# Kernel tuning notes

Hardware: AMD Instinct MI355X
Metric: run time of the kernel (lower is better)

## Reference

```python
import jax, jax.numpy as jnp
import numpy as np

B, H, L, D, S = 4, 16, 4096, 64, 128

def setup_inputs() -> dict:
    key = jax.random.key(0)
    k1, k2 = jax.random.split(key)
    x = jax.random.normal(k1, (B, H, L, D), dtype=jnp.float32)
    c = jax.random.normal(k2, (H, S, D), dtype=jnp.float32)
    # codebook rows are unit-normalized at init (matches torch init)
    c = c / jnp.linalg.norm(c, axis=-1, keepdims=True)
    return {"x": x, "c": c}

def reference(x, c):
    # cosine-similarity scores: [B,H,L,S]
    cos_sim = jnp.einsum('bhld,hsd->bhls', x, c)
    delta_index = jnp.argmax(cos_sim, axis=-1)            # [B,H,L]
    delta_onehot = jax.nn.one_hot(delta_index, c.shape[-2], dtype=jnp.float32)  # [B,H,L,S]
    return (delta_onehot, c)
```

## Files before the change

kernel.cpp:

```cpp
#include <hip/hip_runtime.h>
#include <math.h>

constexpr int BB = 4;
constexpr int HH = 16;
constexpr int LL = 4096;
constexpr int DD = 64;
constexpr int SS = 128;
constexpr int WR = 16;

constexpr float TAU = 2e-3f;

typedef __attribute__((ext_vector_type(8))) short bf16x8;
typedef __attribute__((ext_vector_type(4))) float f32x4;

#define MFMA16 __builtin_amdgcn_mfma_f32_16x16x32_bf16

__device__ __forceinline__ unsigned short f2bf(float v) {
    unsigned u = __float_as_uint(v);
    return (unsigned short)((u + 0x7fffu + ((u >> 16) & 1u)) >> 16);
}

__device__ __forceinline__ void split8(const float4 va, const float4 vb,
                                       uint4* hi, uint4* lo) {
    const float v[8] = {va.x, va.y, va.z, va.w, vb.x, vb.y, vb.z, vb.w};
    unsigned hw[4], lw[4];
    #pragma unroll
    for (int p = 0; p < 4; ++p) {
        const unsigned u0 = __float_as_uint(v[2 * p]);
        const unsigned u1 = __float_as_uint(v[2 * p + 1]);
        const unsigned h0 = u0 & 0xffff0000u;
        const unsigned h1 = u1 & 0xffff0000u;
        hw[p] = (u0 >> 16) | h1;
        lw[p] = (unsigned)f2bf(v[2 * p] - __uint_as_float(h0))
              | ((unsigned)f2bf(v[2 * p + 1] - __uint_as_float(h1)) << 16);
    }
    *hi = make_uint4(hw[0], hw[1], hw[2], hw[3]);
    *lo = make_uint4(lw[0], lw[1], lw[2], lw[3]);
}

union FragU { uint4 q; bf16x8 v; };

__global__ __launch_bounds__(256) void convert_c_kernel(
    const float* __restrict__ c, unsigned char* __restrict__ ws,
    float* __restrict__ out_c)
{
    const int sid = blockIdx.x * 256 + threadIdx.x;
    if (sid == 0) *(int*)(ws + (size_t)HH * 32768) = 0;
    const int h  = sid >> 10;
    const int r  = sid & 1023;
    const int kt = r >> 9;
    const int ct = (r >> 6) & 7;
    const int ln = r & 63;
    const int cc = ct * 16 + (ln & 15);
    const int k0 = kt * 32 + (ln >> 4) * 8;
    const float4* src = (const float4*)(c + ((size_t)h * SS + cc) * DD + k0);
    uint4 hi, lo;
    split8(src[0], src[1], &hi, &lo);
    unsigned char* base =
        ws + (size_t)h * 32768 + (size_t)(((kt << 3) | ct) * 1024 + ln * 16);
    *(uint4*)(base) = hi;
    *(uint4*)(base + 16384) = lo;

    const f32x4* __restrict__ s4 = (const f32x4*)c;
    f32x4* __restrict__ d4 = (f32x4*)out_c;
    __builtin_nontemporal_store(s4[sid], d4 + sid);
    __builtin_nontemporal_store(s4[sid + 16384], d4 + sid + 16384);
}

template <bool USE_WS>
__global__ __launch_bounds__(64, 8) void quantizer_kernel(
    const float* __restrict__ x,
    const float* __restrict__ c,
    const unsigned char* __restrict__ ws,
    float* __restrict__ out,
    int* __restrict__ gcount,
    int* __restrict__ glist)
{
    __shared__ int s_res[WR];

    const int lane = threadIdx.x;
    const int ln15 = lane & 15;
    const long long r0 = (long long)blockIdx.x * WR;
    const int h = (int)((r0 >> 12) & (HH - 1));
    const unsigned char* __restrict__ wsb =
        USE_WS ? (ws + (size_t)h * 32768) : nullptr;
    const float* __restrict__ chead = c + (size_t)h * SS * DD;
    const int k0 = (lane >> 4) * 8;

    bf16x8 af[2][2];
    {
        const float* xr = x + (size_t)(r0 + ln15) * DD + k0;
        #pragma unroll
        for (int kt = 0; kt < 2; ++kt) {
            FragU hi, lo;
            split8(*(const float4*)(xr + kt * 32),
                   *(const float4*)(xr + kt * 32 + 4), &hi.q, &lo.q);
            af[kt][0] = hi.v;
            af[kt][1] = lo.v;
        }
    }

    float m1[4], m2[4];
    int   mi_[4];
    #pragma unroll
    for (int r = 0; r < 4; ++r) {
        m1[r] = -INFINITY; m2[r] = -INFINITY; mi_[r] = 0;
    }

    #pragma unroll 1
    for (int ct = 0; ct < 8; ++ct) {
        f32x4 a0 = {0.f, 0.f, 0.f, 0.f};
        f32x4 a1 = {0.f, 0.f, 0.f, 0.f};
        if constexpr (USE_WS) {
            const unsigned char* bp = wsb + (unsigned)(ct * 1024 + lane * 16);
            {
                const bf16x8 bh = *(const bf16x8*)(bp);
                const bf16x8 bl = *(const bf16x8*)(bp + 16384);
                a0 = MFMA16(af[0][1], bh, a0, 0, 0, 0);
                a0 = MFMA16(af[0][0], bl, a0, 0, 0, 0);
                a0 = MFMA16(af[0][0], bh, a0, 0, 0, 0);
            }
            {
                const bf16x8 bh = *(const bf16x8*)(bp + 8192);
                const bf16x8 bl = *(const bf16x8*)(bp + 24576);
                a1 = MFMA16(af[1][1], bh, a1, 0, 0, 0);
                a1 = MFMA16(af[1][0], bl, a1, 0, 0, 0);
                a1 = MFMA16(af[1][0], bh, a1, 0, 0, 0);
            }
        } else {
            const float* cr = chead + (size_t)(ct * 16 + ln15) * DD + k0;
            {
                FragU bh, bl;
                split8(*(const float4*)cr, *(const float4*)(cr + 4),
                       &bh.q, &bl.q);
                a0 = MFMA16(af[0][1], bh.v, a0, 0, 0, 0);
                a0 = MFMA16(af[0][0], bl.v, a0, 0, 0, 0);
                a0 = MFMA16(af[0][0], bh.v, a0, 0, 0, 0);
            }
            {
                FragU bh, bl;
                split8(*(const float4*)(cr + 32), *(const float4*)(cr + 36),
                       &bh.q, &bl.q);
                a1 = MFMA16(af[1][1], bh.v, a1, 0, 0, 0);
                a1 = MFMA16(af[1][0], bl.v, a1, 0, 0, 0);
                a1 = MFMA16(af[1][0], bh.v, a1, 0, 0, 0);
            }
        }
        #pragma unroll
        for (int r = 0; r < 4; ++r) {
            const float v = a0[r] + a1[r];
            const int col = ct * 16 + ln15;
            m2[r] = __builtin_amdgcn_fmed3f(m1[r], v, m2[r]);
            if (v > m1[r]) { m1[r] = v; mi_[r] = col; }
        }
    }

    {
        int rv[4];
        #pragma unroll
        for (int r = 0; r < 4; ++r) {
            float a1 = m1[r], a2 = m2[r];
            int ai = mi_[r];
            #pragma unroll
            for (int off = 1; off <= 8; off <<= 1) {
                const float o1 = __shfl_xor(a1, off);
                const float o2 = __shfl_xor(a2, off);
                const int   oi = __shfl_xor(ai, off);
                const bool take = (o1 > a1) || (o1 == a1 && oi < ai);
                const float n2 = take ? fmaxf(a1, o2) : fmaxf(a2, o1);
                if (take) { a1 = o1; ai = oi; }
                a2 = n2;
            }
            rv[r] = ai;
            if (ln15 == 0 && (a1 - a2) < TAU) {
                const int row = (lane >> 4) * 4 + r;
                const int p = atomicAdd(gcount, 1);
                glist[p] = (int)(r0 + row);
            }
        }
        if (ln15 == 0)
            *(int4*)&s_res[(lane >> 4) * 4] =
                make_int4(rv[0], rv[1], rv[2], rv[3]);
    }

    f32x4* __restrict__ op = (f32x4*)(out + (size_t)r0 * SS);
    #pragma unroll
    for (int k = 0; k < 8; ++k) {
        const int i = lane + k * 64;
        const int am = s_res[i >> 5];
        const int s0 = (i & 31) * 4;
        f32x4 v = {(s0 + 0 == am) ? 1.f : 0.f,
                   (s0 + 1 == am) ? 1.f : 0.f,
                   (s0 + 2 == am) ? 1.f : 0.f,
                   (s0 + 3 == am) ? 1.f : 0.f};
        __builtin_nontemporal_store(v, op + i);
    }
}

__global__ __launch_bounds__(64) void fixup_kernel(
    const float* __restrict__ x, const float* __restrict__ c,
    const int* __restrict__ gcount, const int* __restrict__ glist,
    float* __restrict__ out)
{
    const int lane = threadIdx.x;
    const int cnt = *gcount;
    for (int idx = blockIdx.x; idx < cnt; idx += gridDim.x) {
        const int row = glist[idx];
        const int h = (row >> 12) & (HH - 1);
        const float* __restrict__ chead = c + (size_t)h * SS * DD;
        const float4* __restrict__ xr = (const float4*)(x + (size_t)row * DD);
        const float4* __restrict__ c0 =
            (const float4*)(chead + (size_t)lane * DD);
        const float4* __restrict__ c1 =
            (const float4*)(chead + (size_t)(lane + 64) * DD);
        float s0 = 0.f, s1 = 0.f;
        #pragma unroll
        for (int q = 0; q < 16; ++q) {
            const float4 a = xr[q];
            const float4 b0 = c0[q];
            const float4 b1 = c1[q];
            s0 = fmaf(a.x, b0.x, s0); s0 = fmaf(a.y, b0.y, s0);
            s0 = fmaf(a.z, b0.z, s0); s0 = fmaf(a.w, b0.w, s0);
            s1 = fmaf(a.x, b1.x, s1); s1 = fmaf(a.y, b1.y, s1);
            s1 = fmaf(a.z, b1.z, s1); s1 = fmaf(a.w, b1.w, s1);
        }
        float v = s0; int bi = lane;
        if (s1 > v) { v = s1; bi = lane + 64; }
        #pragma unroll
        for (int off = 1; off < 64; off <<= 1) {
            const float ov = __shfl_xor(v, off);
            const int   oi = __shfl_xor(bi, off);
            if (ov > v || (ov == v && oi < bi)) { v = ov; bi = oi; }
        }
        f32x4* __restrict__ op = (f32x4*)(out + (size_t)row * SS);
        if (lane < 32) {
            const int s0c = lane * 4;
            f32x4 w = {(s0c + 0 == bi) ? 1.f : 0.f,
                       (s0c + 1 == bi) ? 1.f : 0.f,
                       (s0c + 2 == bi) ? 1.f : 0.f,
                       (s0c + 3 == bi) ? 1.f : 0.f};
            op[lane] = w;
        }
    }
}

extern "C" void kernel_launch(void* const* d_in, const int* in_sizes, int n_in,
                              void* d_out, int out_size, void* d_ws, size_t ws_size,
                              hipStream_t stream) {
    const float* x = (const float*)d_in[0];
    const float* c = (const float*)d_in[1];
    float* out = (float*)d_out;
    float* out_c = out + (size_t)BB * HH * LL * SS;

    const int rows = BB * HH * LL;
    const int blocks = rows / WR;
    const size_t wsB = (size_t)HH * 32768;
    const size_t ws_need = wsB + 64 + (size_t)rows * 4;

    if (d_ws != nullptr && ws_size >= ws_need) {
        unsigned char* wsp = (unsigned char*)d_ws;
        int* gcount = (int*)(wsp + wsB);
        int* glist = (int*)(wsp + wsB + 64);
        convert_c_kernel<<<64, 256, 0, stream>>>(c, wsp, out_c);
        quantizer_kernel<true><<<blocks, 64, 0, stream>>>(
            x, c, wsp, out, gcount, glist);
        fixup_kernel<<<256, 64, 0, stream>>>(x, c, gcount, glist, out);
    } else {
        static int dummy = 0;
        (void)dummy;
        unsigned char* wsp = (unsigned char*)d_ws;
        if (wsp == nullptr || ws_size < 64 + (size_t)rows * 4) {
            fixup_kernel<<<2048, 64, 0, stream>>>(x, c, nullptr, nullptr, out);
            return;
        }
        int* gcount = (int*)wsp;
        int* glist = (int*)(wsp + 64);
        convert_c_kernel<<<64, 256, 0, stream>>>(c, (unsigned char*)wsp, out_c);
        quantizer_kernel<false><<<blocks, 64, 0, stream>>>(
            x, c, nullptr, out, gcount, glist);
        fixup_kernel<<<256, 64, 0, stream>>>(x, c, gcount, glist, out);
    }
}
```

Baseline: 213.1 us.

## Stage codebook in LDS and double-buffer x rows via async global-to-LDS loads

The quantizer kernel now uses 256-thread blocks, each handling 8 groups of 64 rows. The per-head bf16 hi/lo codebook is loaded once into shared memory, so each wave no longer re-reads it from global memory. The x rows are double-buffered into LDS with global_load_lds and an explicit vmcnt wait, so the next group's loads overlap the MFMA and argmax work on the current group. In exchange, far fewer blocks are launched and each uses about 64KB of LDS, which limits occupancy; the hand-placed waitcnt and sched barriers also rely on the exact count of outstanding loads.

```diff
diff --git a/kernel.cpp b/kernel.cpp
--- a/kernel.cpp
+++ b/kernel.cpp
@@ -7,6 +7,8 @@
 constexpr int DD = 64;
 constexpr int SS = 128;
 constexpr int WR = 16;
+constexpr int NW = 4;
+constexpr int NG = 8;
 
 constexpr float TAU = 2e-3f;
 
@@ -68,7 +70,7 @@
 }
 
 template <bool USE_WS>
-__global__ __launch_bounds__(64, 8) void quantizer_kernel(
+__global__ __launch_bounds__(256) void quantizer_kernel(
     const float* __restrict__ x,
     const float* __restrict__ c,
     const unsigned char* __restrict__ ws,
@@ -76,43 +78,99 @@
     int* __restrict__ gcount,
     int* __restrict__ glist)
 {
-    __shared__ int s_res[WR];
-
-    const int lane = threadIdx.x;
+    __shared__ __align__(16) unsigned char smemB[32768];
+    __shared__ __align__(16) unsigned char xstage[NW * 8192];
+    __shared__ int s_res[NW][WR];
+
+    const int tid = threadIdx.x;
+    const int wv = tid >> 6;
+    const int lane = tid & 63;
     const int ln15 = lane & 15;
-    const long long r0 = (long long)blockIdx.x * WR;
-    const int h = (int)((r0 >> 12) & (HH - 1));
-    const unsigned char* __restrict__ wsb =
-        USE_WS ? (ws + (size_t)h * 32768) : nullptr;
+    const long long R0 = (long long)blockIdx.x * (WR * NW * NG);
+    const int h = (int)((R0 >> 12) & (HH - 1));
     const float* __restrict__ chead = c + (size_t)h * SS * DD;
-    const int k0 = (lane >> 4) * 8;
-
-    bf16x8 af[2][2];
-    {
-        const float* xr = x + (size_t)(r0 + ln15) * DD + k0;
+
+    if (USE_WS) {
+        const unsigned char* wsb = ws + (size_t)h * 32768;
+        #pragma unroll
+        for (int it = 0; it < 8; ++it) {
+            const unsigned off = (unsigned)(wv * 8192 + it * 1024);
+            __builtin_amdgcn_global_load_lds(
+                (const __attribute__((address_space(1))) unsigned*)
+                    (wsb + off + (unsigned)(lane * 16)),
+                (__attribute__((address_space(3))) unsigned*)(smemB + off),
+                16, 0, 0);
+        }
+    } else {
+        #pragma unroll
+        for (int it = 0; it < 4; ++it) {
+            const int sid = it * 256 + tid;
+            const int kt = sid >> 9;
+            const int ct = (sid >> 6) & 7;
+            const int ln = sid & 63;
+            const int cc = ct * 16 + (ln & 15);
+            const int k0 = kt * 32 + (ln >> 4) * 8;
+            const float4* src = (const float4*)(chead + (size_t)cc * DD + k0);
+            uint4 hi, lo;
+            split8(src[0], src[1], &hi, &lo);
+            unsigned char* dst = smemB + ((kt << 3) | ct) * 1024 + ln * 16;
+            *(uint4*)dst = hi;
+            *(uint4*)(dst + 16384) = lo;
+        }
+    }
+
+    auto dma_x = [&](int g, int buf) {
+        const long long r0w = R0 + (long long)g * (WR * NW) + wv * WR;
+        const unsigned char* base = (const unsigned char*)(x + (size_t)r0w * DD);
+        unsigned char* dst = xstage + wv * 8192 + buf * 4096;
+        #pragma unroll
+        for (int d = 0; d < 4; ++d) {
+            const int kt = d >> 1, gg = d & 1;
+            const unsigned srcoff = (unsigned)(ln15 * 256 + (lane >> 4) * 32
+                                               + gg * 16 + kt * 128);
+            __builtin_amdgcn_global_load_lds(
+                (const __attribute__((address_space(1))) unsigned*)
+                    (base + srcoff),
+                (__attribute__((address_space(3))) unsigned*)
+                    (dst + d * 1024 + lane * 16),
+                16, 0, 0);
+        }
+    };
+
+    dma_x(0, 0);
+    dma_x(1, 1);
+    __syncthreads();
+
+    #pragma unroll 1
+    for (int g = 0; g < NG; ++g) {
+        asm volatile("s_waitcnt vmcnt(4)" ::: "memory");
+        __builtin_amdgcn_sched_barrier(0);
+
+        const long long r0w = R0 + (long long)g * (WR * NW) + wv * WR;
+        const unsigned char* xb = xstage + wv * 8192 + (g & 1) * 4096;
+
+        bf16x8 af[2][2];
         #pragma unroll
         for (int kt = 0; kt < 2; ++kt) {
+            const float4 va = *(const float4*)(xb + kt * 2048 + lane * 16);
+            const float4 vb = *(const float4*)(xb + kt * 2048 + 1024 + lane * 16);
             FragU hi, lo;
-            split8(*(const float4*)(xr + kt * 32),
-                   *(const float4*)(xr + kt * 32 + 4), &hi.q, &lo.q);
+            split8(va, vb, &hi.q, &lo.q);
             af[kt][0] = hi.v;
             af[kt][1] = lo.v;
         }
-    }
-
-    float m1[4], m2[4];
-    int   mi_[4];
-    #pragma unroll
-    for (int r = 0; r < 4; ++r) {
-        m1[r] = -INFINITY; m2[r] = -INFINITY; mi_[r] = 0;
-    }
-
-    #pragma unroll 1
-    for (int ct = 0; ct < 8; ++ct) {
-        f32x4 a0 = {0.f, 0.f, 0.f, 0.f};
-        f32x4 a1 = {0.f, 0.f, 0.f, 0.f};
-        if constexpr (USE_WS) {
-            const unsigned char* bp = wsb + (unsigned)(ct * 1024 + lane * 16);
+
+        float m1[4], m2[4];
+        int   mi_[4];
+        #pragma unroll
+        for (int r = 0; r < 4; ++r) {
+            m1[r] = -INFINITY; m2[r] = -INFINITY; mi_[r] = 0;
+        }
+        #pragma unroll 2
+        for (int ct = 0; ct < 8; ++ct) {
+            const unsigned char* bp = smemB + (unsigned)(ct * 1024 + lane * 16);
+            f32x4 a0 = {0.f, 0.f, 0.f, 0.f};
+            f32x4 a1 = {0.f, 0.f, 0.f, 0.f};
             {
                 const bf16x8 bh = *(const bf16x8*)(bp);
                 const bf16x8 bl = *(const bf16x8*)(bp + 16384);
@@ -127,73 +185,58 @@
                 a1 = MFMA16(af[1][0], bl, a1, 0, 0, 0);
                 a1 = MFMA16(af[1][0], bh, a1, 0, 0, 0);
             }
-        } else {
-            const float* cr = chead + (size_t)(ct * 16 + ln15) * DD + k0;
-            {
-                FragU bh, bl;
-                split8(*(const float4*)cr, *(const float4*)(cr + 4),
-                       &bh.q, &bl.q);
-                a0 = MFMA16(af[0][1], bh.v, a0, 0, 0, 0);
-                a0 = MFMA16(af[0][0], bl.v, a0, 0, 0, 0);
-                a0 = MFMA16(af[0][0], bh.v, a0, 0, 0, 0);
+            #pragma unroll
+            for (int r = 0; r < 4; ++r) {
+                const float v = a0[r] + a1[r];
+                const int col = ct * 16 + ln15;
+                m2[r] = __builtin_amdgcn_fmed3f(m1[r], v, m2[r]);
+                if (v > m1[r]) { m1[r] = v; mi_[r] = col; }
             }
-            {
-                FragU bh, bl;
-                split8(*(const float4*)(cr + 32), *(const float4*)(cr + 36),
-                       &bh.q, &bl.q);
-                a1 = MFMA16(af[1][1], bh.v, a1, 0, 0, 0);
-                a1 = MFMA16(af[1][0], bl.v, a1, 0, 0, 0);
-                a1 = MFMA16(af[1][0], bh.v, a1, 0, 0, 0);
+        }
+
+        {
+            int rv[4];
+            #pragma unroll
+            for (int r = 0; r < 4; ++r) {
+                float a1 = m1[r], a2 = m2[r];
+                int ai = mi_[r];
+                #pragma unroll
+                for (int off = 1; off <= 8; off <<= 1) {
+                    const float o1 = __shfl_xor(a1, off);
+                    const float o2 = __shfl_xor(a2, off);
+                    const int   oi = __shfl_xor(ai, off);
+                    const bool take = (o1 > a1) || (o1 == a1 && oi < ai);
+                    const float n2 = take ? fmaxf(a1, o2) : fmaxf(a2, o1);
+                    if (take) { a1 = o1; ai = oi; }
+                    a2 = n2;
+                }
+                rv[r] = ai;
+                if (ln15 == 0 && (a1 - a2) < TAU) {
+                    const int row = (lane >> 4) * 4 + r;
+                    const int p = atomicAdd(gcount, 1);
+                    glist[p] = (int)(r0w + row);
+                }
             }
-        }
-        #pragma unroll
-        for (int r = 0; r < 4; ++r) {
-            const float v = a0[r] + a1[r];
-            const int col = ct * 16 + ln15;
-            m2[r] = __builtin_amdgcn_fmed3f(m1[r], v, m2[r]);
-            if (v > m1[r]) { m1[r] = v; mi_[r] = col; }
-        }
-    }
-
-    {
-        int rv[4];
-        #pragma unroll
-        for (int r = 0; r < 4; ++r) {
-            float a1 = m1[r], a2 = m2[r];
-            int ai = mi_[r];
-            #pragma unroll
-            for (int off = 1; off <= 8; off <<= 1) {
-                const float o1 = __shfl_xor(a1, off);
-                const float o2 = __shfl_xor(a2, off);
-                const int   oi = __shfl_xor(ai, off);
-                const bool take = (o1 > a1) || (o1 == a1 && oi < ai);
-                const float n2 = take ? fmaxf(a1, o2) : fmaxf(a2, o1);
-                if (take) { a1 = o1; ai = oi; }
-                a2 = n2;
-            }
-            rv[r] = ai;
-            if (ln15 == 0 && (a1 - a2) < TAU) {
-                const int row = (lane >> 4) * 4 + r;
-                const int p = atomicAdd(gcount, 1);
-                glist[p] = (int)(r0 + row);
-            }
-        }
-        if (ln15 == 0)
-            *(int4*)&s_res[(lane >> 4) * 4] =
-                make_int4(rv[0], rv[1], rv[2], rv[3]);
-    }
-
-    f32x4* __restrict__ op = (f32x4*)(out + (size_t)r0 * SS);
-    #pragma unroll
-    for (int k = 0; k < 8; ++k) {
-        const int i = lane + k * 64;
-        const int am = s_res[i >> 5];
-        const int s0 = (i & 31) * 4;
-        f32x4 v = {(s0 + 0 == am) ? 1.f : 0.f,
-                   (s0 + 1 == am) ? 1.f : 0.f,
-                   (s0 + 2 == am) ? 1.f : 0.f,
-                   (s0 + 3 == am) ? 1.f : 0.f};
-        __builtin_nontemporal_store(v, op + i);
+            if (ln15 == 0)
+                *(int4*)&s_res[wv][(lane >> 4) * 4] =
+                    make_int4(rv[0], rv[1], rv[2], rv[3]);
+        }
+
+        f32x4* __restrict__ op = (f32x4*)(out + (size_t)r0w * SS);
+        #pragma unroll
+        for (int k = 0; k < 8; ++k) {
+            const int i = lane + k * 64;
+            const int am = s_res[wv][i >> 5];
+            const int s0 = (i & 31) * 4;
+            f32x4 v = {(s0 + 0 == am) ? 1.f : 0.f,
+                       (s0 + 1 == am) ? 1.f : 0.f,
+                       (s0 + 2 == am) ? 1.f : 0.f,
+                       (s0 + 3 == am) ? 1.f : 0.f};
+            __builtin_nontemporal_store(v, op + i);
+        }
+
+        __builtin_amdgcn_sched_barrier(0);
+        if (g + 2 < NG) dma_x(g + 2, g & 1);
     }
 }
 
@@ -253,7 +296,7 @@
     float* out_c = out + (size_t)BB * HH * LL * SS;
 
     const int rows = BB * HH * LL;
-    const int blocks = rows / WR;
+    const int blocks = rows / (WR * NW * NG);
     const size_t wsB = (size_t)HH * 32768;
     const size_t ws_need = wsB + 64 + (size_t)rows * 4;
 
@@ -262,22 +305,18 @@
         int* gcount = (int*)(wsp + wsB);
         int* glist = (int*)(wsp + wsB + 64);
         convert_c_kernel<<<64, 256, 0, stream>>>(c, wsp, out_c);
-        quantizer_kernel<true><<<blocks, 64, 0, stream>>>(
+        quantizer_kernel<true><<<blocks, 256, 0, stream>>>(
             x, c, wsp, out, gcount, glist);
         fixup_kernel<<<256, 64, 0, stream>>>(x, c, gcount, glist, out);
-    } else {
-        static int dummy = 0;
-        (void)dummy;
+    } else if (d_ws != nullptr && ws_size >= 64 + (size_t)rows * 4) {
         unsigned char* wsp = (unsigned char*)d_ws;
-        if (wsp == nullptr || ws_size < 64 + (size_t)rows * 4) {
-            fixup_kernel<<<2048, 64, 0, stream>>>(x, c, nullptr, nullptr, out);
-            return;
-        }
         int* gcount = (int*)wsp;
         int* glist = (int*)(wsp + 64);
-        convert_c_kernel<<<64, 256, 0, stream>>>(c, (unsigned char*)wsp, out_c);
-        quantizer_kernel<false><<<blocks, 64, 0, stream>>>(
+        hipMemsetAsync(gcount, 0, 4, stream);
+        quantizer_kernel<false><<<blocks, 256, 0, stream>>>(
             x, c, nullptr, out, gcount, glist);
         fixup_kernel<<<256, 64, 0, stream>>>(x, c, gcount, glist, out);
-    }
-}
+        hipMemcpyAsync(out_c, c, (size_t)HH * SS * DD * sizeof(float),
+                       hipMemcpyDeviceToDevice, stream);
+    }
+}
```

New measurement: 214.3 us. No clear change (+0.5%).
